# Kernel optimization log

Measured on AMD Instinct MI355X. Metric: run time of the kernel, lower is better.

Reference implementation:

```python
import jax, jax.numpy as jnp
import numpy as np
from jax import lax

B, S, V, E, H, NF = 128, 512, 50000, 300, 150, 100  # batch, seq(power of 2), vocab, embed, hidden, filters


def setup_inputs() -> dict:
    key = jax.random.key(0)
    ks = jax.random.split(key, 18)
    p = lambda k, shape, s=0.05: jax.random.normal(k, shape, dtype=jnp.float32) * s
    emb = p(ks[0], (V, E), 0.1).at[0].set(0.0)  # padding_idx=0 row zeroed
    return dict(
        x=jax.random.randint(ks[1], (B, S), 0, V),
        emb=emb,
        w3=p(ks[2], (NF, E, 3)), b3=p(ks[3], (NF,)),
        w4=p(ks[4], (NF, E, 4)), b4=p(ks[5], (NF,)),
        w5=p(ks[6], (NF, E, 5)), b5=p(ks[7], (NF,)),
        Wp=p(ks[8], (H, E + 3 * NF)), bp=p(ks[9], (H,)),
        Wx=p(ks[10], (5 * H, H)), bx=p(ks[11], (5 * H,)),
        UL=p(ks[12], (5 * H, H)), UR=p(ks[13], (5 * H, H)),
        W1=p(ks[14], (H // 2, H)), b1=p(ks[15], (H // 2,)),
        W2=p(ks[16], (3, H // 2)), b2=p(ks[17], (3,)),
    )


def _conv_same(xc, w, b):
    # xc: [B,E,S]; torch Conv1d(padding='same'): left=(k-1)//2, right gets the extra
    k = w.shape[-1]
    pad = ((k - 1) // 2, (k - 1) - (k - 1) // 2)
    y = lax.conv_general_dilated(xc, w, (1,), [pad], dimension_numbers=('NCH', 'OIH', 'NCH'))
    return jax.nn.relu(y + b[None, :, None])


def _cell(gates, lc, rc):
    i, fL, fR, o, u = jnp.split(gates, 5, axis=-1)
    i, fL, fR, o = map(jax.nn.sigmoid, (i, fL, fR, o))
    u = jnp.tanh(u)
    c = i * u
    if lc is not None:
        c = c + fL * lc + fR * rc
    return o * jnp.tanh(c), c


def reference(x, emb, w3, b3, w4, b4, w5, b5, Wp, bp, Wx, bx, UL, UR, W1, b1, W2, b2):
    e = emb[x]                                   # [B,S,E]
    xc = jnp.transpose(e, (0, 2, 1))             # [B,E,S]
    cnn = jnp.concatenate([_conv_same(xc, w3, b3), _conv_same(xc, w4, b4), _conv_same(xc, w5, b5)], axis=1)
    feats = jnp.concatenate([e, jnp.transpose(cnn, (0, 2, 1))], axis=2)  # [B,S,E+3*NF]
    leaf = feats @ Wp.T + bp                     # [B,S,H]
    # Leaves: gates = W_x(feat) + b (no children)
    h, c = _cell(leaf @ Wx.T + bx, None, None)
    # Internal nodes of complete binary tree: x = zeros -> gates = b + U_L h_L + U_R h_R
    n = S
    while n > 1:
        lh, rh = h[:, 0::2], h[:, 1::2]
        lc_, rc_ = c[:, 0::2], c[:, 1::2]
        gates = lh @ UL.T + rh @ UR.T + bx
        h, c = _cell(gates, lc_, rc_)
        n //= 2
    root = h[:, 0]                               # [B,H]
    z = jax.nn.relu(root @ W1.T + b1)            # dropout = identity (eval)
    return z @ W2.T + b2                         # [B,3]
```

## Files before the change

### kernel.cpp

```cpp
#include <hip/hip_runtime.h>
#include <math.h>

#define BB 128
#define SS 512
#define EE 300
#define HH 150
#define TN 16
#define LST 152
#define GS 752
#define UST 752

#define OB_B1   0u
#define OB_B2   1699840u
#define OB_B3   2109440u
#define OB_UT   2416640u
#define OB_BC   3440640u
#define OB_ULT  3442176u
#define OB_URT  3893376u
#define OB_H0   4344576u
#define SZB_HC0 39321600u
#define OB_C0   (OB_H0 + SZB_HC0)
#define OB_H1   (OB_C0 + SZB_HC0)
#define SZB_HC1 19660800u
#define OB_C1   (OB_H1 + SZB_HC1)

#define EST 328
#define CST 328
#define LSU 168
#define AST 332

typedef short s16x8 __attribute__((ext_vector_type(8)));
typedef float f32x4 __attribute__((ext_vector_type(4)));
#define MFMA __builtin_amdgcn_mfma_f32_16x16x32_bf16

typedef unsigned short ushort_t;
typedef unsigned int uint_t;

__device__ __forceinline__ float sigmoidf_(float x) {
    return 1.0f / (1.0f + __expf(-x));
}
__device__ __forceinline__ float tanh_fast(float x) {
    x = fminf(fmaxf(x, -15.0f), 15.0f);
    float e = __expf(2.0f * x);
    return (e - 1.0f) / (e + 1.0f);
}
__device__ __forceinline__ ushort_t f2bf(float f) {
    uint_t u = __float_as_uint(f);
    return (ushort_t)((u + 0x7fffu + ((u >> 16) & 1u)) >> 16);
}
__device__ __forceinline__ void split_bf16(float f, ushort_t& hi, ushort_t& lo) {
    uint_t u = __float_as_uint(f);
    uint_t r = (u + 0x7fffu + ((u >> 16) & 1u)) >> 16;
    hi = (ushort_t)r;
    float d = f - __uint_as_float(r << 16);
    uint_t u2 = __float_as_uint(d);
    uint_t r2 = (u2 + 0x7fffu + ((u2 >> 16) & 1u)) >> 16;
    lo = (ushort_t)r2;
}

__device__ __forceinline__ int b1_tile(int nt, int kt) {
    return (nt < 12) ? nt * 40 + (kt - 10) : 480 + (nt - 12) * 50 + kt;
}

__device__ __forceinline__ void pack_frag(uint_t* out, const ushort_t* hv, const ushort_t* lv) {
    out[0] = hv[0] | (hv[1] << 16); out[1] = hv[2] | (hv[3] << 16);
    out[2] = hv[4] | (hv[5] << 16); out[3] = hv[6] | (hv[7] << 16);
    out[4] = lv[0] | (lv[1] << 16); out[5] = lv[2] | (lv[3] << 16);
    out[6] = lv[4] | (lv[5] << 16); out[7] = lv[6] | (lv[7] << 16);
}

__global__ __launch_bounds__(256) void k_prep(
    const float* __restrict__ w3, const float* __restrict__ b3,
    const float* __restrict__ w4, const float* __restrict__ b4,
    const float* __restrict__ w5, const float* __restrict__ b5,
    const float* __restrict__ Wp, const float* __restrict__ Wx,
    const float* __restrict__ UL, const float* __restrict__ UR,
    char* __restrict__ wsb)
{
    const int W1 = 830 * 64, W2 = 200 * 64, W3 = 150 * 64, WU = 500 * 64;
    int i = blockIdx.x * 256 + threadIdx.x;
    if (i < W1) {
        int T = i >> 6, lane = i & 63;
        int nt, kt;
        if (T < 480) { nt = T / 40; kt = T % 40 + 10; }
        else { int T2 = T - 480; nt = 12 + T2 / 50; kt = T2 % 50; }
        int t = kt / 10, jjb = (kt - t * 10) * 32 + ((lane >> 4) << 3);
        int f = nt * 16 + (lane & 15);
        ushort_t hv[8], lv[8];
        #pragma unroll
        for (int e = 0; e < 8; ++e) {
            int jj = jjb + e;
            float w = 0.0f;
            if (f < 300 && jj < 300) {
                if (f < 100)      { if (t >= 1 && t <= 3) w = w3[f * 900 + jj * 3 + (t - 1)]; }
                else if (f < 200) { if (t >= 1)           w = w4[(f - 100) * 1200 + jj * 4 + (t - 1)]; }
                else              {                       w = w5[(f - 200) * 1500 + jj * 5 + t]; }
            }
            split_bf16(w, hv[e], lv[e]);
        }
        pack_frag((uint_t*)(wsb + OB_B1 + ((size_t)T * 64 + lane) * 32), hv, lv);
        return;
    }
    i -= W1;
    if (i < W2) {
        int T = i >> 6, lane = i & 63;
        int nt = T / 20, kt = T % 20;
        int h = nt * 16 + (lane & 15);
        int kb = kt * 32 + ((lane >> 4) << 3);
        ushort_t hv[8], lv[8];
        #pragma unroll
        for (int e = 0; e < 8; ++e) {
            int k = kb + e;
            float w = 0.0f;
            if (h < 150) {
                if (kt < 10) { if (k < 300) w = Wp[h * 600 + k]; }
                else { int k2 = k - 320; if (k2 < 300) w = Wp[h * 600 + 300 + k2]; }
            }
            split_bf16(w, hv[e], lv[e]);
        }
        pack_frag((uint_t*)(wsb + OB_B2 + ((size_t)T * 64 + lane) * 32), hv, lv);
        return;
    }
    i -= W2;
    if (i < W3) {
        int T = i >> 6, lane = i & 63;
        int nt3 = T / 5, kt = T % 5;
        int g = nt3 / 10, h16 = nt3 % 10;
        int h = h16 * 16 + (lane & 15);
        int kb = kt * 32 + ((lane >> 4) << 3);
        int row = (g == 0 ? 0 : (g == 1 ? 450 : 600)) + h;
        ushort_t hv[8], lv[8];
        #pragma unroll
        for (int e = 0; e < 8; ++e) {
            int k = kb + e;
            float w = (h < 150 && k < 150) ? Wx[row * 150 + k] : 0.0f;
            split_bf16(w, hv[e], lv[e]);
        }
        pack_frag((uint_t*)(wsb + OB_B3 + ((size_t)T * 64 + lane) * 32), hv, lv);
        return;
    }
    i -= W3;
    if (i < WU) {
        int T = i >> 6, lane = i & 63;
        int g = T / 100, rem = T - g * 100;
        int ht = rem / 10, kt = rem - ht * 10;
        int h = ht * 16 + (lane & 15);
        int kb = kt * 32 + ((lane >> 4) << 3);
        ushort_t hv[8], lv[8];
        #pragma unroll
        for (int e = 0; e < 8; ++e) {
            int k = kb + e;
            int half = (k >= 160);
            int j = k - half * 160;
            float w = 0.0f;
            if (h < 150 && j < 150) {
                const float* U = half ? UR : UL;
                w = U[(g * 150 + h) * 150 + j];
            }
            split_bf16(w, hv[e], lv[e]);
        }
        pack_frag((uint_t*)(wsb + OB_UT + ((size_t)T * 64 + lane) * 32), hv, lv);
        return;
    }
    i -= WU;
    if (i < 304) {
        float v = (i < 100) ? b3[i] : (i < 200 ? b4[i - 100] : (i < 300 ? b5[i - 200] : 0.0f));
        ((float*)(wsb + OB_BC))[i] = v;
        return;
    }
    i -= 304;
    if (i < 150 * UST) {
        int j = i / UST, o = i - j * UST;
        ((float*)(wsb + OB_ULT))[i] = (o < 750) ? UL[o * 150 + j] : 0.0f;
        return;
    }
    i -= 150 * UST;
    if (i < 150 * UST) {
        int j = i / UST, o = i - j * UST;
        ((float*)(wsb + OB_URT))[i] = (o < 750) ? UR[o * 150 + j] : 0.0f;
        return;
    }
}

#define LDA(kt_, d0h, d1h) { \
    int t_ = (kt_) / 10; \
    int jj_ = ((kt_) - t_ * 10) * 32 + (lq << 3); \
    int ra_ = lc + t_; \
    d0h = *(const s16x8*)&ehi[ra_ * EST + jj_]; \
    d1h = *(const s16x8*)&ehi[(ra_ + 16) * EST + jj_]; }

__global__ __launch_bounds__(640) void k_leaf(
    const int* __restrict__ x, const float* __restrict__ emb,
    const ushort_t* __restrict__ b1f, const ushort_t* __restrict__ b2f,
    const ushort_t* __restrict__ b3f, const float* __restrict__ bcat,
    const float* __restrict__ bp, const float* __restrict__ bx,
    float* __restrict__ h0, float* __restrict__ c0)
{
    __shared__ ushort_t ehi[36 * EST];
    __shared__ ushort_t chi[32 * CST];
    __shared__ ushort_t lhi[32 * LSU];

    const int b   = blockIdx.x;
    const int s0  = blockIdx.y * 32;
    const int tid = threadIdx.x;
    const int wv  = tid >> 6;
    const int lane = tid & 63;
    const int lc = lane & 15, lq = lane >> 4;

    for (int idx = tid; idx < 36 * 75; idx += 640) {
        int r = idx / 75, q = idx - r * 75;
        int sp = s0 - 2 + r;
        float4 v = make_float4(0.f, 0.f, 0.f, 0.f);
        if (sp >= 0 && sp < SS) {
            int tok = x[b * SS + sp];
            v = *reinterpret_cast<const float4*>(emb + (size_t)tok * EE + q * 4);
        }
        *(ushort4*)&ehi[r * EST + q * 4] =
            make_ushort4(f2bf(v.x), f2bf(v.y), f2bf(v.z), f2bf(v.w));
    }
    for (int idx = tid; idx < 36 * 20; idx += 640) {
        int r = idx / 20, c = 300 + idx % 20;
        ehi[r * EST + c] = 0;
    }
    for (int idx = tid; idx < 32 * 16; idx += 640) {
        int r = idx / 16, c = 304 + idx % 16;
        chi[r * CST + c] = 0;
    }
    __syncthreads();

    {
        const int nt0 = wv;
        const int nt1 = (wv == 9) ? 18 : wv + 10;
        const bool st1 = (wv < 9);
        const int f0 = nt0 * 16 + lc;
        const int f1 = nt1 * 16 + lc;
        const float bv0 = bcat[f0];
        const float bv1 = st1 ? bcat[f1] : 0.0f;
        const f32x4 z4 = {0.f, 0.f, 0.f, 0.f};
        f32x4 s00a = {bv0, bv0, bv0, bv0}, s00b = z4;
        f32x4 s01a = s00a,                 s01b = z4;
        f32x4 s10a = {bv1, bv1, bv1, bv1}, s10b = z4;
        f32x4 s11a = s10a,                 s11b = z4;

        if (nt1 >= 12) {
            #pragma unroll
            for (int kt = 0; kt < 10; ++kt) {
                const ushort_t* p8 = b1f + ((size_t)b1_tile(nt1, kt) * 64 + lane) * 16;
                s16x8 Bh = *(const s16x8*)p8;
                s16x8 Bl = *(const s16x8*)(p8 + 8);
                int jj = kt * 32 + (lq << 3);
                s16x8 A0h = *(const s16x8*)&ehi[lc * EST + jj];
                s16x8 A1h = *(const s16x8*)&ehi[(lc + 16) * EST + jj];
                s10a = MFMA(A0h, Bh, s10a, 0, 0, 0);
                s10b = MFMA(A0h, Bl, s10b, 0, 0, 0);
                s11a = MFMA(A1h, Bh, s11a, 0, 0, 0);
                s11b = MFMA(A1h, Bl, s11b, 0, 0, 0);
            }
        }

        const ushort_t* p;
        p = b1f + ((size_t)b1_tile(nt0, 10) * 64 + lane) * 16;
        s16x8 Bha0 = *(const s16x8*)p, Bla0 = *(const s16x8*)(p + 8);
        p = b1f + ((size_t)b1_tile(nt1, 10) * 64 + lane) * 16;
        s16x8 Bha1 = *(const s16x8*)p, Bla1 = *(const s16x8*)(p + 8);
        p = b1f + ((size_t)b1_tile(nt0, 11) * 64 + lane) * 16;
        s16x8 Bhb0 = *(const s16x8*)p, Blb0 = *(const s16x8*)(p + 8);
        p = b1f + ((size_t)b1_tile(nt1, 11) * 64 + lane) * 16;
        s16x8 Bhb1 = *(const s16x8*)p, Blb1 = *(const s16x8*)(p + 8);

        s16x8 Pa0h, Pa1h, Pb0h, Pb1h;
        LDA(10, Pa0h, Pa1h);
        LDA(11, Pb0h, Pb1h);

        for (int kt = 10; kt < 50; kt += 2) {
            int k2 = (kt + 2 < 50) ? kt + 2 : 10;
            p = b1f + ((size_t)b1_tile(nt0, k2) * 64 + lane) * 16;
            s16x8 nha0 = *(const s16x8*)p, nla0 = *(const s16x8*)(p + 8);
            p = b1f + ((size_t)b1_tile(nt1, k2) * 64 + lane) * 16;
            s16x8 nha1 = *(const s16x8*)p, nla1 = *(const s16x8*)(p + 8);

            s00a = MFMA(Pa0h, Bha0, s00a, 0, 0, 0);
            s00b = MFMA(Pa0h, Bla0, s00b, 0, 0, 0);
            s01a = MFMA(Pa1h, Bha0, s01a, 0, 0, 0);
            s01b = MFMA(Pa1h, Bla0, s01b, 0, 0, 0);
            s10a = MFMA(Pa0h, Bha1, s10a, 0, 0, 0);
            s10b = MFMA(Pa0h, Bla1, s10b, 0, 0, 0);
            s11a = MFMA(Pa1h, Bha1, s11a, 0, 0, 0);
            s11b = MFMA(Pa1h, Bla1, s11b, 0, 0, 0);

            LDA(k2, Pa0h, Pa1h);

            int k3 = (kt + 3 < 50) ? kt + 3 : 11;
            p = b1f + ((size_t)b1_tile(nt0, k3) * 64 + lane) * 16;
            s16x8 nhb0 = *(const s16x8*)p, nlb0 = *(const s16x8*)(p + 8);
            p = b1f + ((size_t)b1_tile(nt1, k3) * 64 + lane) * 16;
            s16x8 nhb1 = *(const s16x8*)p, nlb1 = *(const s16x8*)(p + 8);

            s00a = MFMA(Pb0h, Bhb0, s00a, 0, 0, 0);
            s00b = MFMA(Pb0h, Blb0, s00b, 0, 0, 0);
            s01a = MFMA(Pb1h, Bhb0, s01a, 0, 0, 0);
            s01b = MFMA(Pb1h, Blb0, s01b, 0, 0, 0);
            s10a = MFMA(Pb0h, Bhb1, s10a, 0, 0, 0);
            s10b = MFMA(Pb0h, Blb1, s10b, 0, 0, 0);
            s11a = MFMA(Pb1h, Bhb1, s11a, 0, 0, 0);
            s11b = MFMA(Pb1h, Blb1, s11b, 0, 0, 0);

            LDA(k3, Pb0h, Pb1h);

            Bha0 = nha0; Bla0 = nla0; Bha1 = nha1; Bla1 = nla1;
            Bhb0 = nhb0; Blb0 = nlb0; Bhb1 = nhb1; Blb1 = nlb1;
        }

        f32x4 c00 = s00a + s00b;
        f32x4 c01 = s01a + s01b;
        f32x4 c10 = s10a + s10b;
        f32x4 c11 = s11a + s11b;

        #pragma unroll
        for (int r = 0; r < 4; ++r) {
            int pp = lq * 4 + r;
            chi[pp * CST + f0]        = f2bf(fmaxf(c00[r], 0.0f));
            chi[(pp + 16) * CST + f0] = f2bf(fmaxf(c01[r], 0.0f));
            if (st1) {
                chi[pp * CST + f1]        = f2bf(fmaxf(c10[r], 0.0f));
                chi[(pp + 16) * CST + f1] = f2bf(fmaxf(c11[r], 0.0f));
            }
        }
    }
    __syncthreads();

    {
        const int hcol = wv * 16 + lc;
        const float bv = (hcol < 150) ? bp[hcol] : 0.0f;
        const f32x4 z4 = {0.f, 0.f, 0.f, 0.f};
        f32x4 d0a = {bv, bv, bv, bv}, d0b = z4;
        f32x4 d1a = d0a,              d1b = z4;
        #pragma unroll
        for (int kt = 0; kt < 20; ++kt) {
            s16x8 A0h, A1h;
            if (kt < 10) {
                int col = kt * 32 + (lq << 3);
                int ra = lc + 2;
                A0h = *(const s16x8*)&ehi[ra * EST + col];
                A1h = *(const s16x8*)&ehi[(ra + 16) * EST + col];
            } else {
                int col = (kt - 10) * 32 + (lq << 3);
                A0h = *(const s16x8*)&chi[lc * CST + col];
                A1h = *(const s16x8*)&chi[(lc + 16) * CST + col];
            }
            const ushort_t* p8 = b2f + ((size_t)(wv * 20 + kt) * 64 + lane) * 16;
            s16x8 Bh = *(const s16x8*)p8;
            s16x8 Bl = *(const s16x8*)(p8 + 8);
            d0a = MFMA(A0h, Bh, d0a, 0, 0, 0);
            d0b = MFMA(A0h, Bl, d0b, 0, 0, 0);
            d1a = MFMA(A1h, Bh, d1a, 0, 0, 0);
            d1b = MFMA(A1h, Bl, d1b, 0, 0, 0);
        }
        f32x4 d0 = d0a + d0b;
        f32x4 d1 = d1a + d1b;
        #pragma unroll
        for (int r = 0; r < 4; ++r) {
            int pp = lq * 4 + r;
            lhi[pp * LSU + hcol]        = f2bf(d0[r]);
            lhi[(pp + 16) * LSU + hcol] = f2bf(d1[r]);
        }
    }
    __syncthreads();

    {
        const int hc = wv * 16 + lc;
        const bool hval = (hc < 150);
        const float bi = hval ? bx[hc] : 0.0f;
        const float bo = hval ? bx[450 + hc] : 0.0f;
        const float bu = hval ? bx[600 + hc] : 0.0f;
        const f32x4 z4 = {0.f, 0.f, 0.f, 0.f};
        f32x4 gi0a = {bi, bi, bi, bi}, gi0b = z4, gi1a = gi0a, gi1b = z4;
        f32x4 go0a = {bo, bo, bo, bo}, go0b = z4, go1a = go0a, go1b = z4;
        f32x4 gu0a = {bu, bu, bu, bu}, gu0b = z4, gu1a = gu0a, gu1b = z4;
        #pragma unroll
        for (int kt = 0; kt < 5; ++kt) {
            int col = kt * 32 + (lq << 3);
            s16x8 A0h = *(const s16x8*)&lhi[lc * LSU + col];
            s16x8 A1h = *(const s16x8*)&lhi[(lc + 16) * LSU + col];
            const ushort_t* p8i = b3f + ((size_t)((0 + wv) * 5 + kt) * 64 + lane) * 16;
            const ushort_t* p8o = b3f + ((size_t)((10 + wv) * 5 + kt) * 64 + lane) * 16;
            const ushort_t* p8u = b3f + ((size_t)((20 + wv) * 5 + kt) * 64 + lane) * 16;
            s16x8 Bh, Bl;
            Bh = *(const s16x8*)p8i; Bl = *(const s16x8*)(p8i + 8);
            gi0a = MFMA(A0h, Bh, gi0a, 0, 0, 0); gi0b = MFMA(A0h, Bl, gi0b, 0, 0, 0);
            gi1a = MFMA(A1h, Bh, gi1a, 0, 0, 0); gi1b = MFMA(A1h, Bl, gi1b, 0, 0, 0);
            Bh = *(const s16x8*)p8o; Bl = *(const s16x8*)(p8o + 8);
            go0a = MFMA(A0h, Bh, go0a, 0, 0, 0); go0b = MFMA(A0h, Bl, go0b, 0, 0, 0);
            go1a = MFMA(A1h, Bh, go1a, 0, 0, 0); go1b = MFMA(A1h, Bl, go1b, 0, 0, 0);
            Bh = *(const s16x8*)p8u; Bl = *(const s16x8*)(p8u + 8);
            gu0a = MFMA(A0h, Bh, gu0a, 0, 0, 0); gu0b = MFMA(A0h, Bl, gu0b, 0, 0, 0);
            gu1a = MFMA(A1h, Bh, gu1a, 0, 0, 0); gu1b = MFMA(A1h, Bl, gu1b, 0, 0, 0);
        }
        if (hval) {
            f32x4 gi0 = gi0a + gi0b, gi1 = gi1a + gi1b;
            f32x4 go0 = go0a + go0b, go1 = go1a + go1b;
            f32x4 gu0 = gu0a + gu0b, gu1 = gu1a + gu1b;
            #pragma unroll
            for (int r = 0; r < 4; ++r) {
                {
                    int s = s0 + lq * 4 + r;
                    float iv = sigmoidf_(gi0[r]), ov = sigmoidf_(go0[r]), uv = tanh_fast(gu0[r]);
                    float cc = iv * uv;
                    float hh = ov * tanh_fast(cc);
                    size_t o = ((size_t)b * SS + s) * HH + hc;
                    h0[o] = hh;
                    c0[o] = cc;
                }
                {
                    int s = s0 + 16 + lq * 4 + r;
                    float iv = sigmoidf_(gi1[r]), ov = sigmoidf_(go1[r]), uv = tanh_fast(gu1[r]);
                    float cc = iv * uv;
                    float hh = ov * tanh_fast(cc);
                    size_t o = ((size_t)b * SS + s) * HH + hc;
                    h0[o] = hh;
                    c0[o] = cc;
                }
            }
        }
    }
}

__global__ __launch_bounds__(640) void k_tree2(
    const float* __restrict__ in_h, const float* __restrict__ in_c,
    float* __restrict__ out_h, float* __restrict__ out_c,
    int n_out,
    const ushort_t* __restrict__ utf, const float* __restrict__ bx)
{
    __shared__ ushort_t ahi[32 * AST], alo[32 * AST];

    const int b   = blockIdx.x;
    const int m0  = blockIdx.y * 32;
    const int tid = threadIdx.x;
    const int wv  = tid >> 6, lane = tid & 63;
    const int lc  = lane & 15, lq = lane >> 4;
    const int n_in = n_out * 2;

    const float* src = in_h + ((size_t)b * n_in + 2 * m0) * HH;
    for (int idx = tid; idx < 4800; idx += 640) {
        float2 v = *(const float2*)(src + idx * 2);
        int e = idx * 2;
        int r = e / 150, k = e - r * 150;
        int base = (r >> 1) * AST + (r & 1) * 160 + k;
        ushort_t ha, la, hb, lb;
        split_bf16(v.x, ha, la);
        split_bf16(v.y, hb, lb);
        ahi[base] = ha; ahi[base + 1] = hb;
        alo[base] = la; alo[base + 1] = lb;
    }
    {
        int m = tid / 20, j = tid - (tid / 20) * 20;
        int k = (j < 10) ? (150 + j) : (310 + j - 10);
        ahi[m * AST + k] = 0; alo[m * AST + k] = 0;
    }
    __syncthreads();

    const int hc = wv * 16 + lc;
    const bool hval = (hc < 150);
    const float bi = hval ? bx[hc] : 0.f;
    const float bl = hval ? bx[150 + hc] : 0.f;
    const float br = hval ? bx[300 + hc] : 0.f;
    const float bo = hval ? bx[450 + hc] : 0.f;
    const float bu = hval ? bx[600 + hc] : 0.f;
    f32x4 ai0 = {bi, bi, bi, bi}, ai1 = ai0;
    f32x4 al0 = {bl, bl, bl, bl}, al1 = al0;
    f32x4 ar0 = {br, br, br, br}, ar1 = ar0;
    f32x4 ao0 = {bo, bo, bo, bo}, ao1 = ao0;
    f32x4 au0 = {bu, bu, bu, bu}, au1 = au0;

    const size_t gstride = (size_t)100 * 1024;
    for (int kt = 0; kt < 10; ++kt) {
        int col = kt * 32 + (lq << 3);
        s16x8 A0h = *(const s16x8*)&ahi[lc * AST + col];
        s16x8 A0l = *(const s16x8*)&alo[lc * AST + col];
        s16x8 A1h = *(const s16x8*)&ahi[(lc + 16) * AST + col];
        s16x8 A1l = *(const s16x8*)&alo[(lc + 16) * AST + col];
        const ushort_t* pb = utf + ((size_t)(wv * 10 + kt) * 64 + lane) * 16;
        s16x8 Bh, Bl;
        Bh = *(const s16x8*)pb; Bl = *(const s16x8*)(pb + 8);
        ai0 = MFMA(A0h, Bh, ai0, 0, 0, 0); ai0 = MFMA(A0h, Bl, ai0, 0, 0, 0); ai0 = MFMA(A0l, Bh, ai0, 0, 0, 0);
        ai1 = MFMA(A1h, Bh, ai1, 0, 0, 0); ai1 = MFMA(A1h, Bl, ai1, 0, 0, 0); ai1 = MFMA(A1l, Bh, ai1, 0, 0, 0);
        pb += gstride;
        Bh = *(const s16x8*)pb; Bl = *(const s16x8*)(pb + 8);
        al0 = MFMA(A0h, Bh, al0, 0, 0, 0); al0 = MFMA(A0h, Bl, al0, 0, 0, 0); al0 = MFMA(A0l, Bh, al0, 0, 0, 0);
        al1 = MFMA(A1h, Bh, al1, 0, 0, 0); al1 = MFMA(A1h, Bl, al1, 0, 0, 0); al1 = MFMA(A1l, Bh, al1, 0, 0, 0);
        pb += gstride;
        Bh = *(const s16x8*)pb; Bl = *(const s16x8*)(pb + 8);
        ar0 = MFMA(A0h, Bh, ar0, 0, 0, 0); ar0 = MFMA(A0h, Bl, ar0, 0, 0, 0); ar0 = MFMA(A0l, Bh, ar0, 0, 0, 0);
        ar1 = MFMA(A1h, Bh, ar1, 0, 0, 0); ar1 = MFMA(A1h, Bl, ar1, 0, 0, 0); ar1 = MFMA(A1l, Bh, ar1, 0, 0, 0);
        pb += gstride;
        Bh = *(const s16x8*)pb; Bl = *(const s16x8*)(pb + 8);
        ao0 = MFMA(A0h, Bh, ao0, 0, 0, 0); ao0 = MFMA(A0h, Bl, ao0, 0, 0, 0); ao0 = MFMA(A0l, Bh, ao0, 0, 0, 0);
        ao1 = MFMA(A1h, Bh, ao1, 0, 0, 0); ao1 = MFMA(A1h, Bl, ao1, 0, 0, 0); ao1 = MFMA(A1l, Bh, ao1, 0, 0, 0);
        pb += gstride;
        Bh = *(const s16x8*)pb; Bl = *(const s16x8*)(pb + 8);
        au0 = MFMA(A0h, Bh, au0, 0, 0, 0); au0 = MFMA(A0h, Bl, au0, 0, 0, 0); au0 = MFMA(A0l, Bh, au0, 0, 0, 0);
        au1 = MFMA(A1h, Bh, au1, 0, 0, 0); au1 = MFMA(A1h, Bl, au1, 0, 0, 0); au1 = MFMA(A1l, Bh, au1, 0, 0, 0);
    }

    if (hval) {
        #pragma unroll
        for (int r = 0; r < 4; ++r) {
            int ml = lq * 4 + r;
            {
                int m = m0 + ml;
                size_t cb = ((size_t)b * n_in + 2 * m) * HH + hc;
                float iv = sigmoidf_(ai0[r]);
                float fl = sigmoidf_(al0[r]);
                float fr = sigmoidf_(ar0[r]);
                float ov = sigmoidf_(ao0[r]);
                float uv = tanh_fast(au0[r]);
                float cc = iv * uv + fl * in_c[cb] + fr * in_c[cb + HH];
                size_t ob = ((size_t)b * n_out + m) * HH + hc;
                out_h[ob] = ov * tanh_fast(cc);
                out_c[ob] = cc;
            }
            {
                int m = m0 + 16 + ml;
                size_t cb = ((size_t)b * n_in + 2 * m) * HH + hc;
                float iv = sigmoidf_(ai1[r]);
                float fl = sigmoidf_(al1[r]);
                float fr = sigmoidf_(ar1[r]);
                float ov = sigmoidf_(ao1[r]);
                float uv = tanh_fast(au1[r]);
                float cc = iv * uv + fl * in_c[cb] + fr * in_c[cb + HH];
                size_t ob = ((size_t)b * n_out + m) * HH + hc;
                out_h[ob] = ov * tanh_fast(cc);
                out_c[ob] = cc;
            }
        }
    }
}

template<int NN>
__device__ __forceinline__ void tail_level(
    const float* curh, const float* curc, float* nxth, float* nxtc, float* gs,
    const float* ul1, const float* ur1, float bx1, int o1, bool ov_, int tid)
{
    __syncthreads();
    if (ov_) {
        float a1[NN];
        #pragma unroll
        for (int m = 0; m < NN; ++m) a1[m] = bx1;
        for (int j = 0; j < 150; j += 2) {
            int r0 = j * UST, r1 = (j + 1) * UST;
            float wl1a = ul1[r0], wl1b = ul1[r1];
            float wr1a = ur1[r0], wr1b = ur1[r1];
            #pragma unroll
            for (int m = 0; m < NN; ++m) {
                float2 lv = *(const float2*)(curh + (2 * m) * LST + j);
                float2 rv = *(const float2*)(curh + (2 * m + 1) * LST + j);
                a1[m] += lv.x * wl1a + lv.y * wl1b + rv.x * wr1a + rv.y * wr1b;
            }
        }
        #pragma unroll
        for (int m = 0; m < NN; ++m) gs[m * GS + o1] = a1[m];
    }
    __syncthreads();
    for (int idx = tid; idx < NN * HH; idx += 768) {
        int m = idx / HH, h = idx - m * HH;
        float iv = sigmoidf_(gs[m * GS + h]);
        float fL = sigmoidf_(gs[m * GS + 150 + h]);
        float fR = sigmoidf_(gs[m * GS + 300 + h]);
        float ov = sigmoidf_(gs[m * GS + 450 + h]);
        float uv = tanh_fast(gs[m * GS + 600 + h]);
        float cc = iv * uv + fL * curc[2 * m * LST + h] + fR * curc[(2 * m + 1) * LST + h];
        nxth[m * LST + h] = ov * tanh_fast(cc);
        nxtc[m * LST + h] = cc;
    }
}

__global__ __launch_bounds__(768) void k_tail(
    const float* __restrict__ in_h, const float* __restrict__ in_c,
    const float* __restrict__ ULT, const float* __restrict__ URT,
    const float* __restrict__ bx,
    const float* __restrict__ W1, const float* __restrict__ b1,
    const float* __restrict__ W2, const float* __restrict__ b2,
    float* __restrict__ out)
{
    __shared__ float pool[96 * LST + TN * GS];
    float* Ah = pool;
    float* Ac = Ah + 32 * LST;
    float* Bh = Ac + 32 * LST;
    float* Bc = Bh + 16 * LST;
    float* gs = Bc + 16 * LST;
    __shared__ float z_s[80];

    const int b   = blockIdx.x;
    const int tid = threadIdx.x;

    for (int idx = tid; idx < 32 * HH; idx += 768) {
        int p = idx / HH, j = idx - p * HH;
        size_t base = ((size_t)b * 32 + p) * HH + j;
        Ah[p * LST + j] = in_h[base];
        Ac[p * LST + j] = in_c[base];
    }

    const int o1 = tid;
    const bool ov_ = (o1 < 750);
    const float bx1 = ov_ ? bx[o1] : 0.0f;
    const float* ul1 = ULT + (ov_ ? o1 : 0);
    const float* ur1 = URT + (ov_ ? o1 : 0);

    tail_level<16>(Ah, Ac, Bh, Bc, gs, ul1, ur1, bx1, o1, ov_, tid);
    tail_level<8 >(Bh, Bc, Ah, Ac, gs, ul1, ur1, bx1, o1, ov_, tid);
    tail_level<4 >(Ah, Ac, Bh, Bc, gs, ul1, ur1, bx1, o1, ov_, tid);
    tail_level<2 >(Bh, Bc, Ah, Ac, gs, ul1, ur1, bx1, o1, ov_, tid);
    tail_level<1 >(Ah, Ac, Bh, Bc, gs, ul1, ur1, bx1, o1, ov_, tid);
    __syncthreads();

    if (tid < 75) {
        const float* w = W1 + (size_t)tid * 150;
        float acc = b1[tid];
        for (int j = 0; j < 150; ++j) acc += Bh[j] * w[j];
        z_s[tid] = fmaxf(acc, 0.0f);
    }
    __syncthreads();
    if (tid < 3) {
        const float* w = W2 + (size_t)tid * 75;
        float acc = b2[tid];
        for (int j = 0; j < 75; ++j) acc += z_s[j] * w[j];
        out[(size_t)b * 3 + tid] = acc;
    }
}

extern "C" void kernel_launch(void* const* d_in, const int* in_sizes, int n_in,
                              void* d_out, int out_size, void* d_ws, size_t ws_size,
                              hipStream_t stream) {
    const int*   x   = (const int*)  d_in[0];
    const float* emb = (const float*)d_in[1];
    const float* w3  = (const float*)d_in[2];
    const float* b3  = (const float*)d_in[3];
    const float* w4  = (const float*)d_in[4];
    const float* b4  = (const float*)d_in[5];
    const float* w5  = (const float*)d_in[6];
    const float* b5  = (const float*)d_in[7];
    const float* Wp  = (const float*)d_in[8];
    const float* bp  = (const float*)d_in[9];
    const float* Wx  = (const float*)d_in[10];
    const float* bx  = (const float*)d_in[11];
    const float* UL  = (const float*)d_in[12];
    const float* UR  = (const float*)d_in[13];
    const float* W1  = (const float*)d_in[14];
    const float* b1  = (const float*)d_in[15];
    const float* W2  = (const float*)d_in[16];
    const float* b2  = (const float*)d_in[17];
    float* out = (float*)d_out;

    char* wsb = (char*)d_ws;
    const ushort_t* b1f = (const ushort_t*)(wsb + OB_B1);
    const ushort_t* b2f = (const ushort_t*)(wsb + OB_B2);
    const ushort_t* b3f = (const ushort_t*)(wsb + OB_B3);
    const ushort_t* utf = (const ushort_t*)(wsb + OB_UT);
    const float* bcat = (const float*)(wsb + OB_BC);
    const float* ULT  = (const float*)(wsb + OB_ULT);
    const float* URT  = (const float*)(wsb + OB_URT);
    float* h0 = (float*)(wsb + OB_H0);
    float* c0 = (float*)(wsb + OB_C0);
    float* h1 = (float*)(wsb + OB_H1);
    float* c1 = (float*)(wsb + OB_C1);

    {
        int total = 830 * 64 + 200 * 64 + 150 * 64 + 500 * 64 + 304 + 2 * 150 * UST;
        k_prep<<<(total + 255) / 256, 256, 0, stream>>>(
            w3, b3, w4, b4, w5, b5, Wp, Wx, UL, UR, wsb);
    }

    k_leaf<<<dim3(BB, SS / 32), 640, 0, stream>>>(
        x, emb, b1f, b2f, b3f, bcat, bp, bx, h0, c0);

    k_tree2<<<dim3(BB, 8), 640, 0, stream>>>(h0, c0, h1, c1, 256, utf, bx);
    k_tree2<<<dim3(BB, 4), 640, 0, stream>>>(h1, c1, h0, c0, 128, utf, bx);
    k_tree2<<<dim3(BB, 2), 640, 0, stream>>>(h0, c0, h1, c1,  64, utf, bx);
    k_tree2<<<dim3(BB, 1), 640, 0, stream>>>(h1, c1, h0, c0,  32, utf, bx);

    k_tail<<<BB, 768, 0, stream>>>(h0, c0, ULT, URT, bx, W1, b1, W2, b2, out);
}
```

Measured before the change: 570.2 us.

## Fuse six tree levels into one kernel per 64-leaf subtree with LDS-resident state

Replaces four per-level k_tree2 launches with a single k_treef kernel. Each block reduces a 64-leaf subtree through six levels, from 32 nodes down to 1, keeping h (as bf16 hi/lo split) and c in shared memory between levels. Only the 8 subtree roots per batch go to global memory, and k_tail now starts from 8 nodes instead of 32. This removes launch overhead and global round-trips of intermediate h/c. In exchange, the deeper levels run with mostly idle waves (n<16 still pays a full 16-row MFMA tile) and only 1024 blocks, all serialized within each block.

Result: slower. 630.1 us (+10.5%).

```diff
diff --git a/kernel.cpp b/kernel.cpp
--- a/kernel.cpp
+++ b/kernel.cpp
@@ -21,8 +21,6 @@
 #define SZB_HC0 39321600u
 #define OB_C0   (OB_H0 + SZB_HC0)
 #define OB_H1   (OB_C0 + SZB_HC0)
-#define SZB_HC1 19660800u
-#define OB_C1   (OB_H1 + SZB_HC1)
 
 #define EST 328
 #define CST 328
@@ -425,39 +423,42 @@
     }
 }
 
-__global__ __launch_bounds__(640) void k_tree2(
-    const float* __restrict__ in_h, const float* __restrict__ in_c,
-    float* __restrict__ out_h, float* __restrict__ out_c,
-    int n_out,
+__global__ __launch_bounds__(640) void k_treef(
+    const float* __restrict__ h0, const float* __restrict__ c0,
+    float* __restrict__ hr, float* __restrict__ cr,
     const ushort_t* __restrict__ utf, const float* __restrict__ bx)
 {
-    __shared__ ushort_t ahi[32 * AST], alo[32 * AST];
-
-    const int b   = blockIdx.x;
-    const int m0  = blockIdx.y * 32;
+    __shared__ ushort_t Ab0h[32 * AST], Ab0l[32 * AST];
+    __shared__ ushort_t Ab1h[16 * AST], Ab1l[16 * AST];
+    __shared__ float cb0[32 * 152], cb1[16 * 152];
+
+    const int b = blockIdx.x, g = blockIdx.y;
     const int tid = threadIdx.x;
-    const int wv  = tid >> 6, lane = tid & 63;
-    const int lc  = lane & 15, lq = lane >> 4;
-    const int n_in = n_out * 2;
-
-    const float* src = in_h + ((size_t)b * n_in + 2 * m0) * HH;
+    const int wv = tid >> 6, lane = tid & 63;
+    const int lc = lane & 15, lq = lane >> 4;
+
+    const float* src = h0 + (size_t)(b * 512 + g * 64) * HH;
     for (int idx = tid; idx < 4800; idx += 640) {
         float2 v = *(const float2*)(src + idx * 2);
         int e = idx * 2;
         int r = e / 150, k = e - r * 150;
         int base = (r >> 1) * AST + (r & 1) * 160 + k;
-        ushort_t ha, la, hb, lb;
+        ushort_t ha, la, hb2, lb2;
         split_bf16(v.x, ha, la);
-        split_bf16(v.y, hb, lb);
-        ahi[base] = ha; ahi[base + 1] = hb;
-        alo[base] = la; alo[base + 1] = lb;
+        split_bf16(v.y, hb2, lb2);
+        Ab0h[base] = ha; Ab0h[base + 1] = hb2;
+        Ab0l[base] = la; Ab0l[base + 1] = lb2;
     }
     {
         int m = tid / 20, j = tid - (tid / 20) * 20;
         int k = (j < 10) ? (150 + j) : (310 + j - 10);
-        ahi[m * AST + k] = 0; alo[m * AST + k] = 0;
-    }
-    __syncthreads();
+        Ab0h[m * AST + k] = 0; Ab0l[m * AST + k] = 0;
+        if (m < 16) { Ab1h[m * AST + k] = 0; Ab1l[m * AST + k] = 0; }
+    }
+    __syncthreads();
+
+    const size_t gb = (size_t)(b * 512 + g * 64) * HH;
+    const size_t go = (size_t)(b * 8 + g) * HH;
 
     const int hc = wv * 16 + lc;
     const bool hval = (hc < 150);
@@ -466,73 +467,84 @@
     const float br = hval ? bx[300 + hc] : 0.f;
     const float bo = hval ? bx[450 + hc] : 0.f;
     const float bu = hval ? bx[600 + hc] : 0.f;
-    f32x4 ai0 = {bi, bi, bi, bi}, ai1 = ai0;
-    f32x4 al0 = {bl, bl, bl, bl}, al1 = al0;
-    f32x4 ar0 = {br, br, br, br}, ar1 = ar0;
-    f32x4 ao0 = {bo, bo, bo, bo}, ao1 = ao0;
-    f32x4 au0 = {bu, bu, bu, bu}, au1 = au0;
-
     const size_t gstride = (size_t)100 * 1024;
-    for (int kt = 0; kt < 10; ++kt) {
-        int col = kt * 32 + (lq << 3);
-        s16x8 A0h = *(const s16x8*)&ahi[lc * AST + col];
-        s16x8 A0l = *(const s16x8*)&alo[lc * AST + col];
-        s16x8 A1h = *(const s16x8*)&ahi[(lc + 16) * AST + col];
-        s16x8 A1l = *(const s16x8*)&alo[(lc + 16) * AST + col];
-        const ushort_t* pb = utf + ((size_t)(wv * 10 + kt) * 64 + lane) * 16;
-        s16x8 Bh, Bl;
-        Bh = *(const s16x8*)pb; Bl = *(const s16x8*)(pb + 8);
-        ai0 = MFMA(A0h, Bh, ai0, 0, 0, 0); ai0 = MFMA(A0h, Bl, ai0, 0, 0, 0); ai0 = MFMA(A0l, Bh, ai0, 0, 0, 0);
-        ai1 = MFMA(A1h, Bh, ai1, 0, 0, 0); ai1 = MFMA(A1h, Bl, ai1, 0, 0, 0); ai1 = MFMA(A1l, Bh, ai1, 0, 0, 0);
-        pb += gstride;
-        Bh = *(const s16x8*)pb; Bl = *(const s16x8*)(pb + 8);
-        al0 = MFMA(A0h, Bh, al0, 0, 0, 0); al0 = MFMA(A0h, Bl, al0, 0, 0, 0); al0 = MFMA(A0l, Bh, al0, 0, 0, 0);
-        al1 = MFMA(A1h, Bh, al1, 0, 0, 0); al1 = MFMA(A1h, Bl, al1, 0, 0, 0); al1 = MFMA(A1l, Bh, al1, 0, 0, 0);
-        pb += gstride;
-        Bh = *(const s16x8*)pb; Bl = *(const s16x8*)(pb + 8);
-        ar0 = MFMA(A0h, Bh, ar0, 0, 0, 0); ar0 = MFMA(A0h, Bl, ar0, 0, 0, 0); ar0 = MFMA(A0l, Bh, ar0, 0, 0, 0);
-        ar1 = MFMA(A1h, Bh, ar1, 0, 0, 0); ar1 = MFMA(A1h, Bl, ar1, 0, 0, 0); ar1 = MFMA(A1l, Bh, ar1, 0, 0, 0);
-        pb += gstride;
-        Bh = *(const s16x8*)pb; Bl = *(const s16x8*)(pb + 8);
-        ao0 = MFMA(A0h, Bh, ao0, 0, 0, 0); ao0 = MFMA(A0h, Bl, ao0, 0, 0, 0); ao0 = MFMA(A0l, Bh, ao0, 0, 0, 0);
-        ao1 = MFMA(A1h, Bh, ao1, 0, 0, 0); ao1 = MFMA(A1h, Bl, ao1, 0, 0, 0); ao1 = MFMA(A1l, Bh, ao1, 0, 0, 0);
-        pb += gstride;
-        Bh = *(const s16x8*)pb; Bl = *(const s16x8*)(pb + 8);
-        au0 = MFMA(A0h, Bh, au0, 0, 0, 0); au0 = MFMA(A0h, Bl, au0, 0, 0, 0); au0 = MFMA(A0l, Bh, au0, 0, 0, 0);
-        au1 = MFMA(A1h, Bh, au1, 0, 0, 0); au1 = MFMA(A1h, Bl, au1, 0, 0, 0); au1 = MFMA(A1l, Bh, au1, 0, 0, 0);
-    }
-
-    if (hval) {
-        #pragma unroll
-        for (int r = 0; r < 4; ++r) {
-            int ml = lq * 4 + r;
-            {
-                int m = m0 + ml;
-                size_t cb = ((size_t)b * n_in + 2 * m) * HH + hc;
-                float iv = sigmoidf_(ai0[r]);
-                float fl = sigmoidf_(al0[r]);
-                float fr = sigmoidf_(ar0[r]);
-                float ov = sigmoidf_(ao0[r]);
-                float uv = tanh_fast(au0[r]);
-                float cc = iv * uv + fl * in_c[cb] + fr * in_c[cb + HH];
-                size_t ob = ((size_t)b * n_out + m) * HH + hc;
-                out_h[ob] = ov * tanh_fast(cc);
-                out_c[ob] = cc;
-            }
-            {
-                int m = m0 + 16 + ml;
-                size_t cb = ((size_t)b * n_in + 2 * m) * HH + hc;
-                float iv = sigmoidf_(ai1[r]);
-                float fl = sigmoidf_(al1[r]);
-                float fr = sigmoidf_(ar1[r]);
-                float ov = sigmoidf_(ao1[r]);
-                float uv = tanh_fast(au1[r]);
-                float cc = iv * uv + fl * in_c[cb] + fr * in_c[cb + HH];
-                size_t ob = ((size_t)b * n_out + m) * HH + hc;
-                out_h[ob] = ov * tanh_fast(cc);
-                out_c[ob] = cc;
-            }
-        }
+
+    const ushort_t* Ah = Ab0h;  const ushort_t* Al = Ab0l;
+    ushort_t* Aoh = Ab1h;       ushort_t* Aol = Ab1l;
+    const float* cin = cb1;
+    float* cout = cb0;
+
+    for (int n = 32; n >= 1; n >>= 1) {
+        const int nmt = (n + 15) >> 4;
+        for (int mt = 0; mt < nmt; ++mt) {
+            f32x4 ai  = {bi, bi, bi, bi};
+            f32x4 afl = {bl, bl, bl, bl};
+            f32x4 afr = {br, br, br, br};
+            f32x4 ao  = {bo, bo, bo, bo};
+            f32x4 au  = {bu, bu, bu, bu};
+            const int arow = mt * 16 + lc;
+            for (int kt = 0; kt < 10; ++kt) {
+                int col = kt * 32 + (lq << 3);
+                s16x8 A0h = *(const s16x8*)&Ah[arow * AST + col];
+                s16x8 A0l = *(const s16x8*)&Al[arow * AST + col];
+                const ushort_t* pb = utf + ((size_t)(wv * 10 + kt) * 64 + lane) * 16;
+                s16x8 Bh, Bl;
+                Bh = *(const s16x8*)pb; Bl = *(const s16x8*)(pb + 8);
+                ai = MFMA(A0h, Bh, ai, 0, 0, 0); ai = MFMA(A0h, Bl, ai, 0, 0, 0); ai = MFMA(A0l, Bh, ai, 0, 0, 0);
+                pb += gstride;
+                Bh = *(const s16x8*)pb; Bl = *(const s16x8*)(pb + 8);
+                afl = MFMA(A0h, Bh, afl, 0, 0, 0); afl = MFMA(A0h, Bl, afl, 0, 0, 0); afl = MFMA(A0l, Bh, afl, 0, 0, 0);
+                pb += gstride;
+                Bh = *(const s16x8*)pb; Bl = *(const s16x8*)(pb + 8);
+                afr = MFMA(A0h, Bh, afr, 0, 0, 0); afr = MFMA(A0h, Bl, afr, 0, 0, 0); afr = MFMA(A0l, Bh, afr, 0, 0, 0);
+                pb += gstride;
+                Bh = *(const s16x8*)pb; Bl = *(const s16x8*)(pb + 8);
+                ao = MFMA(A0h, Bh, ao, 0, 0, 0); ao = MFMA(A0h, Bl, ao, 0, 0, 0); ao = MFMA(A0l, Bh, ao, 0, 0, 0);
+                pb += gstride;
+                Bh = *(const s16x8*)pb; Bl = *(const s16x8*)(pb + 8);
+                au = MFMA(A0h, Bh, au, 0, 0, 0); au = MFMA(A0h, Bl, au, 0, 0, 0); au = MFMA(A0l, Bh, au, 0, 0, 0);
+            }
+            if (hval) {
+                #pragma unroll
+                for (int r = 0; r < 4; ++r) {
+                    int pnode = mt * 16 + lq * 4 + r;
+                    if (pnode < n) {
+                        float lcc, rcc;
+                        if (n == 32) {
+                            size_t cb2 = gb + (size_t)(2 * pnode) * HH + hc;
+                            lcc = c0[cb2];
+                            rcc = c0[cb2 + HH];
+                        } else {
+                            lcc = cin[(2 * pnode) * 152 + hc];
+                            rcc = cin[(2 * pnode + 1) * 152 + hc];
+                        }
+                        float iv = sigmoidf_(ai[r]);
+                        float fl = sigmoidf_(afl[r]);
+                        float fr = sigmoidf_(afr[r]);
+                        float ov = sigmoidf_(ao[r]);
+                        float uv = tanh_fast(au[r]);
+                        float cc = iv * uv + fl * lcc + fr * rcc;
+                        float hh = ov * tanh_fast(cc);
+                        if (n > 1) {
+                            cout[pnode * 152 + hc] = cc;
+                            ushort_t hu, lu2;
+                            split_bf16(hh, hu, lu2);
+                            int ab = (pnode >> 1) * AST + (pnode & 1) * 160 + hc;
+                            Aoh[ab] = hu; Aol[ab] = lu2;
+                        } else {
+                            hr[go + hc] = hh;
+                            cr[go + hc] = cc;
+                        }
+                    }
+                }
+            }
+        }
+        {
+            const ushort_t* th = Ah; Ah = Aoh; Aoh = (ushort_t*)th;
+            const ushort_t* tl = Al; Al = Aol; Aol = (ushort_t*)tl;
+            const float* tc = cin; cin = cout; cout = (float*)tc;
+        }
+        __syncthreads();
     }
 }
 
@@ -574,30 +586,30 @@
     }
 }
 
-__global__ __launch_bounds__(768) void k_tail(
-    const float* __restrict__ in_h, const float* __restrict__ in_c,
+__global__ __launch_bounds__(768) void k_tail8(
+    const float* __restrict__ hr, const float* __restrict__ cr,
     const float* __restrict__ ULT, const float* __restrict__ URT,
     const float* __restrict__ bx,
     const float* __restrict__ W1, const float* __restrict__ b1,
     const float* __restrict__ W2, const float* __restrict__ b2,
     float* __restrict__ out)
 {
-    __shared__ float pool[96 * LST + TN * GS];
+    __shared__ float pool[8 * LST + 8 * LST + 4 * LST + 4 * LST + 4 * GS];
     float* Ah = pool;
-    float* Ac = Ah + 32 * LST;
-    float* Bh = Ac + 32 * LST;
-    float* Bc = Bh + 16 * LST;
-    float* gs = Bc + 16 * LST;
+    float* Ac = Ah + 8 * LST;
+    float* Bh = Ac + 8 * LST;
+    float* Bc = Bh + 4 * LST;
+    float* gs = Bc + 4 * LST;
     __shared__ float z_s[80];
 
     const int b   = blockIdx.x;
     const int tid = threadIdx.x;
 
-    for (int idx = tid; idx < 32 * HH; idx += 768) {
+    for (int idx = tid; idx < 8 * HH; idx += 768) {
         int p = idx / HH, j = idx - p * HH;
-        size_t base = ((size_t)b * 32 + p) * HH + j;
-        Ah[p * LST + j] = in_h[base];
-        Ac[p * LST + j] = in_c[base];
+        size_t base = ((size_t)b * 8 + p) * HH + j;
+        Ah[p * LST + j] = hr[base];
+        Ac[p * LST + j] = cr[base];
     }
 
     const int o1 = tid;
@@ -606,11 +618,9 @@
     const float* ul1 = ULT + (ov_ ? o1 : 0);
     const float* ur1 = URT + (ov_ ? o1 : 0);
 
-    tail_level<16>(Ah, Ac, Bh, Bc, gs, ul1, ur1, bx1, o1, ov_, tid);
-    tail_level<8 >(Bh, Bc, Ah, Ac, gs, ul1, ur1, bx1, o1, ov_, tid);
-    tail_level<4 >(Ah, Ac, Bh, Bc, gs, ul1, ur1, bx1, o1, ov_, tid);
-    tail_level<2 >(Bh, Bc, Ah, Ac, gs, ul1, ur1, bx1, o1, ov_, tid);
-    tail_level<1 >(Ah, Ac, Bh, Bc, gs, ul1, ur1, bx1, o1, ov_, tid);
+    tail_level<4>(Ah, Ac, Bh, Bc, gs, ul1, ur1, bx1, o1, ov_, tid);
+    tail_level<2>(Bh, Bc, Ah, Ac, gs, ul1, ur1, bx1, o1, ov_, tid);
+    tail_level<1>(Ah, Ac, Bh, Bc, gs, ul1, ur1, bx1, o1, ov_, tid);
     __syncthreads();
 
     if (tid < 75) {
@@ -661,8 +671,8 @@
     const float* URT  = (const float*)(wsb + OB_URT);
     float* h0 = (float*)(wsb + OB_H0);
     float* c0 = (float*)(wsb + OB_C0);
-    float* h1 = (float*)(wsb + OB_H1);
-    float* c1 = (float*)(wsb + OB_C1);
+    float* hr = (float*)(wsb + OB_H1);
+    float* cr = hr + (size_t)BB * 8 * HH;
 
     {
         int total = 830 * 64 + 200 * 64 + 150 * 64 + 500 * 64 + 304 + 2 * 150 * UST;
@@ -673,10 +683,7 @@
     k_leaf<<<dim3(BB, SS / 32), 640, 0, stream>>>(
         x, emb, b1f, b2f, b3f, bcat, bp, bx, h0, c0);
 
-    k_tree2<<<dim3(BB, 8), 640, 0, stream>>>(h0, c0, h1, c1, 256, utf, bx);
-    k_tree2<<<dim3(BB, 4), 640, 0, stream>>>(h1, c1, h0, c0, 128, utf, bx);
-    k_tree2<<<dim3(BB, 2), 640, 0, stream>>>(h0, c0, h1, c1,  64, utf, bx);
-    k_tree2<<<dim3(BB, 1), 640, 0, stream>>>(h1, c1, h0, c0,  32, utf, bx);
-
-    k_tail<<<BB, 768, 0, stream>>>(h0, c0, ULT, URT, bx, W1, b1, W2, b2, out);
-}
+    k_treef<<<dim3(BB, 8), 640, 0, stream>>>(h0, c0, hr, cr, utf, bx);
+
+    k_tail8<<<BB, 768, 0, stream>>>(hr, cr, ULT, URT, bx, W1, b1, W2, b2, out);
+}
```

## Fuse pairs of tree levels into one kernel using LDS for intermediates

Applied to the files above, without the earlier changes.

Each tree kernel now computes two consecutive binary-tree levels. The intermediate h is kept in shared memory as split bf16 and c is kept in fp32 in shared memory, instead of round-tripping through global memory. This halves the number of tree launches and removes the global writes and reads of the intermediate levels. In exchange it uses more LDS per block, and the second stage runs with only half the MFMA row tiles active.

New measurement: 675.1 us. 1.18x slower.

```diff
diff --git a/kernel.cpp b/kernel.cpp
--- a/kernel.cpp
+++ b/kernel.cpp
@@ -425,20 +425,23 @@
     }
 }
 
-__global__ __launch_bounds__(640) void k_tree2(
+__global__ __launch_bounds__(640) void k_tree2p(
     const float* __restrict__ in_h, const float* __restrict__ in_c,
     float* __restrict__ out_h, float* __restrict__ out_c,
-    int n_out,
+    int n_out1,
     const ushort_t* __restrict__ utf, const float* __restrict__ bx)
 {
     __shared__ ushort_t ahi[32 * AST], alo[32 * AST];
+    __shared__ ushort_t a2h[16 * AST], a2l[16 * AST];
+    __shared__ float cb[32 * 152];
 
     const int b   = blockIdx.x;
     const int m0  = blockIdx.y * 32;
     const int tid = threadIdx.x;
     const int wv  = tid >> 6, lane = tid & 63;
     const int lc  = lane & 15, lq = lane >> 4;
-    const int n_in = n_out * 2;
+    const int n_in = n_out1 * 2;
+    const int n_out2 = n_out1 >> 1;
 
     const float* src = in_h + ((size_t)b * n_in + 2 * m0) * HH;
     for (int idx = tid; idx < 4800; idx += 640) {
@@ -456,6 +459,7 @@
         int m = tid / 20, j = tid - (tid / 20) * 20;
         int k = (j < 10) ? (150 + j) : (310 + j - 10);
         ahi[m * AST + k] = 0; alo[m * AST + k] = 0;
+        if (m < 16) { a2h[m * AST + k] = 0; a2l[m * AST + k] = 0; }
     }
     __syncthreads();
 
@@ -466,70 +470,131 @@
     const float br = hval ? bx[300 + hc] : 0.f;
     const float bo = hval ? bx[450 + hc] : 0.f;
     const float bu = hval ? bx[600 + hc] : 0.f;
-    f32x4 ai0 = {bi, bi, bi, bi}, ai1 = ai0;
-    f32x4 al0 = {bl, bl, bl, bl}, al1 = al0;
-    f32x4 ar0 = {br, br, br, br}, ar1 = ar0;
-    f32x4 ao0 = {bo, bo, bo, bo}, ao1 = ao0;
-    f32x4 au0 = {bu, bu, bu, bu}, au1 = au0;
-
     const size_t gstride = (size_t)100 * 1024;
-    for (int kt = 0; kt < 10; ++kt) {
-        int col = kt * 32 + (lq << 3);
-        s16x8 A0h = *(const s16x8*)&ahi[lc * AST + col];
-        s16x8 A0l = *(const s16x8*)&alo[lc * AST + col];
-        s16x8 A1h = *(const s16x8*)&ahi[(lc + 16) * AST + col];
-        s16x8 A1l = *(const s16x8*)&alo[(lc + 16) * AST + col];
-        const ushort_t* pb = utf + ((size_t)(wv * 10 + kt) * 64 + lane) * 16;
-        s16x8 Bh, Bl;
-        Bh = *(const s16x8*)pb; Bl = *(const s16x8*)(pb + 8);
-        ai0 = MFMA(A0h, Bh, ai0, 0, 0, 0); ai0 = MFMA(A0h, Bl, ai0, 0, 0, 0); ai0 = MFMA(A0l, Bh, ai0, 0, 0, 0);
-        ai1 = MFMA(A1h, Bh, ai1, 0, 0, 0); ai1 = MFMA(A1h, Bl, ai1, 0, 0, 0); ai1 = MFMA(A1l, Bh, ai1, 0, 0, 0);
-        pb += gstride;
-        Bh = *(const s16x8*)pb; Bl = *(const s16x8*)(pb + 8);
-        al0 = MFMA(A0h, Bh, al0, 0, 0, 0); al0 = MFMA(A0h, Bl, al0, 0, 0, 0); al0 = MFMA(A0l, Bh, al0, 0, 0, 0);
-        al1 = MFMA(A1h, Bh, al1, 0, 0, 0); al1 = MFMA(A1h, Bl, al1, 0, 0, 0); al1 = MFMA(A1l, Bh, al1, 0, 0, 0);
-        pb += gstride;
-        Bh = *(const s16x8*)pb; Bl = *(const s16x8*)(pb + 8);
-        ar0 = MFMA(A0h, Bh, ar0, 0, 0, 0); ar0 = MFMA(A0h, Bl, ar0, 0, 0, 0); ar0 = MFMA(A0l, Bh, ar0, 0, 0, 0);
-        ar1 = MFMA(A1h, Bh, ar1, 0, 0, 0); ar1 = MFMA(A1h, Bl, ar1, 0, 0, 0); ar1 = MFMA(A1l, Bh, ar1, 0, 0, 0);
-        pb += gstride;
-        Bh = *(const s16x8*)pb; Bl = *(const s16x8*)(pb + 8);
-        ao0 = MFMA(A0h, Bh, ao0, 0, 0, 0); ao0 = MFMA(A0h, Bl, ao0, 0, 0, 0); ao0 = MFMA(A0l, Bh, ao0, 0, 0, 0);
-        ao1 = MFMA(A1h, Bh, ao1, 0, 0, 0); ao1 = MFMA(A1h, Bl, ao1, 0, 0, 0); ao1 = MFMA(A1l, Bh, ao1, 0, 0, 0);
-        pb += gstride;
-        Bh = *(const s16x8*)pb; Bl = *(const s16x8*)(pb + 8);
-        au0 = MFMA(A0h, Bh, au0, 0, 0, 0); au0 = MFMA(A0h, Bl, au0, 0, 0, 0); au0 = MFMA(A0l, Bh, au0, 0, 0, 0);
-        au1 = MFMA(A1h, Bh, au1, 0, 0, 0); au1 = MFMA(A1h, Bl, au1, 0, 0, 0); au1 = MFMA(A1l, Bh, au1, 0, 0, 0);
-    }
-
-    if (hval) {
-        #pragma unroll
-        for (int r = 0; r < 4; ++r) {
-            int ml = lq * 4 + r;
-            {
-                int m = m0 + ml;
-                size_t cb = ((size_t)b * n_in + 2 * m) * HH + hc;
-                float iv = sigmoidf_(ai0[r]);
-                float fl = sigmoidf_(al0[r]);
-                float fr = sigmoidf_(ar0[r]);
-                float ov = sigmoidf_(ao0[r]);
-                float uv = tanh_fast(au0[r]);
-                float cc = iv * uv + fl * in_c[cb] + fr * in_c[cb + HH];
-                size_t ob = ((size_t)b * n_out + m) * HH + hc;
-                out_h[ob] = ov * tanh_fast(cc);
-                out_c[ob] = cc;
-            }
-            {
-                int m = m0 + 16 + ml;
-                size_t cb = ((size_t)b * n_in + 2 * m) * HH + hc;
-                float iv = sigmoidf_(ai1[r]);
-                float fl = sigmoidf_(al1[r]);
-                float fr = sigmoidf_(ar1[r]);
-                float ov = sigmoidf_(ao1[r]);
-                float uv = tanh_fast(au1[r]);
-                float cc = iv * uv + fl * in_c[cb] + fr * in_c[cb + HH];
-                size_t ob = ((size_t)b * n_out + m) * HH + hc;
-                out_h[ob] = ov * tanh_fast(cc);
+
+    {
+        f32x4 ai0 = {bi, bi, bi, bi}, ai1 = ai0;
+        f32x4 al0 = {bl, bl, bl, bl}, al1 = al0;
+        f32x4 ar0 = {br, br, br, br}, ar1 = ar0;
+        f32x4 ao0 = {bo, bo, bo, bo}, ao1 = ao0;
+        f32x4 au0 = {bu, bu, bu, bu}, au1 = au0;
+
+        for (int kt = 0; kt < 10; ++kt) {
+            int col = kt * 32 + (lq << 3);
+            s16x8 A0h = *(const s16x8*)&ahi[lc * AST + col];
+            s16x8 A0l = *(const s16x8*)&alo[lc * AST + col];
+            s16x8 A1h = *(const s16x8*)&ahi[(lc + 16) * AST + col];
+            s16x8 A1l = *(const s16x8*)&alo[(lc + 16) * AST + col];
+            const ushort_t* pb = utf + ((size_t)(wv * 10 + kt) * 64 + lane) * 16;
+            s16x8 Bh, Bl;
+            Bh = *(const s16x8*)pb; Bl = *(const s16x8*)(pb + 8);
+            ai0 = MFMA(A0h, Bh, ai0, 0, 0, 0); ai0 = MFMA(A0h, Bl, ai0, 0, 0, 0); ai0 = MFMA(A0l, Bh, ai0, 0, 0, 0);
+            ai1 = MFMA(A1h, Bh, ai1, 0, 0, 0); ai1 = MFMA(A1h, Bl, ai1, 0, 0, 0); ai1 = MFMA(A1l, Bh, ai1, 0, 0, 0);
+            pb += gstride;
+            Bh = *(const s16x8*)pb; Bl = *(const s16x8*)(pb + 8);
+            al0 = MFMA(A0h, Bh, al0, 0, 0, 0); al0 = MFMA(A0h, Bl, al0, 0, 0, 0); al0 = MFMA(A0l, Bh, al0, 0, 0, 0);
+            al1 = MFMA(A1h, Bh, al1, 0, 0, 0); al1 = MFMA(A1h, Bl, al1, 0, 0, 0); al1 = MFMA(A1l, Bh, al1, 0, 0, 0);
+            pb += gstride;
+            Bh = *(const s16x8*)pb; Bl = *(const s16x8*)(pb + 8);
+            ar0 = MFMA(A0h, Bh, ar0, 0, 0, 0); ar0 = MFMA(A0h, Bl, ar0, 0, 0, 0); ar0 = MFMA(A0l, Bh, ar0, 0, 0, 0);
+            ar1 = MFMA(A1h, Bh, ar1, 0, 0, 0); ar1 = MFMA(A1h, Bl, ar1, 0, 0, 0); ar1 = MFMA(A1l, Bh, ar1, 0, 0, 0);
+            pb += gstride;
+            Bh = *(const s16x8*)pb; Bl = *(const s16x8*)(pb + 8);
+            ao0 = MFMA(A0h, Bh, ao0, 0, 0, 0); ao0 = MFMA(A0h, Bl, ao0, 0, 0, 0); ao0 = MFMA(A0l, Bh, ao0, 0, 0, 0);
+            ao1 = MFMA(A1h, Bh, ao1, 0, 0, 0); ao1 = MFMA(A1h, Bl, ao1, 0, 0, 0); ao1 = MFMA(A1l, Bh, ao1, 0, 0, 0);
+            pb += gstride;
+            Bh = *(const s16x8*)pb; Bl = *(const s16x8*)(pb + 8);
+            au0 = MFMA(A0h, Bh, au0, 0, 0, 0); au0 = MFMA(A0h, Bl, au0, 0, 0, 0); au0 = MFMA(A0l, Bh, au0, 0, 0, 0);
+            au1 = MFMA(A1h, Bh, au1, 0, 0, 0); au1 = MFMA(A1h, Bl, au1, 0, 0, 0); au1 = MFMA(A1l, Bh, au1, 0, 0, 0);
+        }
+
+        if (hval) {
+            #pragma unroll
+            for (int r = 0; r < 4; ++r) {
+                int ml = lq * 4 + r;
+                {
+                    int pnode = ml;
+                    int m = m0 + pnode;
+                    size_t cbg = ((size_t)b * n_in + 2 * m) * HH + hc;
+                    float iv = sigmoidf_(ai0[r]);
+                    float fl = sigmoidf_(al0[r]);
+                    float fr = sigmoidf_(ar0[r]);
+                    float ov = sigmoidf_(ao0[r]);
+                    float uv = tanh_fast(au0[r]);
+                    float cc = iv * uv + fl * in_c[cbg] + fr * in_c[cbg + HH];
+                    float hh = ov * tanh_fast(cc);
+                    cb[pnode * 152 + hc] = cc;
+                    ushort_t hu, lu2;
+                    split_bf16(hh, hu, lu2);
+                    int ab = (pnode >> 1) * AST + (pnode & 1) * 160 + hc;
+                    a2h[ab] = hu; a2l[ab] = lu2;
+                }
+                {
+                    int pnode = 16 + ml;
+                    int m = m0 + pnode;
+                    size_t cbg = ((size_t)b * n_in + 2 * m) * HH + hc;
+                    float iv = sigmoidf_(ai1[r]);
+                    float fl = sigmoidf_(al1[r]);
+                    float fr = sigmoidf_(ar1[r]);
+                    float ov = sigmoidf_(ao1[r]);
+                    float uv = tanh_fast(au1[r]);
+                    float cc = iv * uv + fl * in_c[cbg] + fr * in_c[cbg + HH];
+                    float hh = ov * tanh_fast(cc);
+                    cb[pnode * 152 + hc] = cc;
+                    ushort_t hu, lu2;
+                    split_bf16(hh, hu, lu2);
+                    int ab = (pnode >> 1) * AST + (pnode & 1) * 160 + hc;
+                    a2h[ab] = hu; a2l[ab] = lu2;
+                }
+            }
+        }
+    }
+    __syncthreads();
+
+    {
+        f32x4 ai = {bi, bi, bi, bi};
+        f32x4 al = {bl, bl, bl, bl};
+        f32x4 ar = {br, br, br, br};
+        f32x4 ao = {bo, bo, bo, bo};
+        f32x4 au = {bu, bu, bu, bu};
+
+        for (int kt = 0; kt < 10; ++kt) {
+            int col = kt * 32 + (lq << 3);
+            s16x8 A0h = *(const s16x8*)&a2h[lc * AST + col];
+            s16x8 A0l = *(const s16x8*)&a2l[lc * AST + col];
+            const ushort_t* pb = utf + ((size_t)(wv * 10 + kt) * 64 + lane) * 16;
+            s16x8 Bh, Bl;
+            Bh = *(const s16x8*)pb; Bl = *(const s16x8*)(pb + 8);
+            ai = MFMA(A0h, Bh, ai, 0, 0, 0); ai = MFMA(A0h, Bl, ai, 0, 0, 0); ai = MFMA(A0l, Bh, ai, 0, 0, 0);
+            pb += gstride;
+            Bh = *(const s16x8*)pb; Bl = *(const s16x8*)(pb + 8);
+            al = MFMA(A0h, Bh, al, 0, 0, 0); al = MFMA(A0h, Bl, al, 0, 0, 0); al = MFMA(A0l, Bh, al, 0, 0, 0);
+            pb += gstride;
+            Bh = *(const s16x8*)pb; Bl = *(const s16x8*)(pb + 8);
+            ar = MFMA(A0h, Bh, ar, 0, 0, 0); ar = MFMA(A0h, Bl, ar, 0, 0, 0); ar = MFMA(A0l, Bh, ar, 0, 0, 0);
+            pb += gstride;
+            Bh = *(const s16x8*)pb; Bl = *(const s16x8*)(pb + 8);
+            ao = MFMA(A0h, Bh, ao, 0, 0, 0); ao = MFMA(A0h, Bl, ao, 0, 0, 0); ao = MFMA(A0l, Bh, ao, 0, 0, 0);
+            pb += gstride;
+            Bh = *(const s16x8*)pb; Bl = *(const s16x8*)(pb + 8);
+            au = MFMA(A0h, Bh, au, 0, 0, 0); au = MFMA(A0h, Bl, au, 0, 0, 0); au = MFMA(A0l, Bh, au, 0, 0, 0);
+        }
+
+        if (hval) {
+            #pragma unroll
+            for (int r = 0; r < 4; ++r) {
+                int node = lq * 4 + r;
+                float lcc = cb[(2 * node) * 152 + hc];
+                float rcc = cb[(2 * node + 1) * 152 + hc];
+                float iv = sigmoidf_(ai[r]);
+                float fl = sigmoidf_(al[r]);
+                float fr = sigmoidf_(ar[r]);
+                float ov = sigmoidf_(ao[r]);
+                float uv = tanh_fast(au[r]);
+                float cc = iv * uv + fl * lcc + fr * rcc;
+                float hh = ov * tanh_fast(cc);
+                size_t ob = ((size_t)b * n_out2 + blockIdx.y * 16 + node) * HH + hc;
+                out_h[ob] = hh;
                 out_c[ob] = cc;
             }
         }
@@ -662,7 +727,7 @@
     float* h0 = (float*)(wsb + OB_H0);
     float* c0 = (float*)(wsb + OB_C0);
     float* h1 = (float*)(wsb + OB_H1);
-    float* c1 = (float*)(wsb + OB_C1);
+    float* c1 = h1 + (size_t)BB * 256 * HH;
 
     {
         int total = 830 * 64 + 200 * 64 + 150 * 64 + 500 * 64 + 304 + 2 * 150 * UST;
@@ -673,10 +738,8 @@
     k_leaf<<<dim3(BB, SS / 32), 640, 0, stream>>>(
         x, emb, b1f, b2f, b3f, bcat, bp, bx, h0, c0);
 
-    k_tree2<<<dim3(BB, 8), 640, 0, stream>>>(h0, c0, h1, c1, 256, utf, bx);
-    k_tree2<<<dim3(BB, 4), 640, 0, stream>>>(h1, c1, h0, c0, 128, utf, bx);
-    k_tree2<<<dim3(BB, 2), 640, 0, stream>>>(h0, c0, h1, c1,  64, utf, bx);
-    k_tree2<<<dim3(BB, 1), 640, 0, stream>>>(h1, c1, h0, c0,  32, utf, bx);
+    k_tree2p<<<dim3(BB, 8), 640, 0, stream>>>(h0, c0, h1, c1, 256, utf, bx);
+    k_tree2p<<<dim3(BB, 2), 640, 0, stream>>>(h1, c1, h0, c0, 64, utf, bx);
 
     k_tail<<<BB, 768, 0, stream>>>(h0, c0, ULT, URT, bx, W1, b1, W2, b2, out);
 }
```
